# Kernel tuning notes

Measured on AMD Instinct MI355X. Metric: run time of the kernel, lower is better.

Reference implementation:

```python
import jax, jax.numpy as jnp
import numpy as np

TAU = 2.0       # spikingjelly LIFNode default tau
V_TH = 1.0      # default v_threshold
T_STEPS = 16
MAX_ACTION = 1.0
ALPHA = 4.0     # surrogate.Sigmoid default alpha

@jax.custom_vjp
def spike(x):
    # Heaviside(v - v_th) with sigmoid surrogate gradient
    return (x >= 0).astype(x.dtype)

def _spike_fwd(x):
    return spike(x), x

def _spike_bwd(x, g):
    s = jax.nn.sigmoid(ALPHA * x)
    return (g * ALPHA * s * (1.0 - s),)

spike.defvjp(_spike_fwd, _spike_bwd)

def setup_inputs() -> dict:
    key = jax.random.key(0)
    ks = jax.random.split(key, 7)
    B, S, H, A = 131072, 128, 256, 8
    def lin(k, out_d, in_d):
        return jax.random.normal(k, (out_d, in_d), jnp.float32) / np.sqrt(in_d)
    return {
        "state": jax.random.normal(ks[0], (B, S), jnp.float32),
        "W1": lin(ks[1], H, S),
        "b1": jax.random.normal(ks[2], (H,), jnp.float32) * 0.1,
        "W2": lin(ks[3], H, H),
        "b2": jax.random.normal(ks[4], (H,), jnp.float32) * 0.1,
        "W3": lin(ks[5], A, H),
        "b3": jax.random.normal(ks[6], (A,), jnp.float32) * 0.1,
    }

def reference(state, W1, b1, W2, b2, W3, b3):
    B = state.shape[0]
    H, A = W1.shape[0], W3.shape[0]
    # input current to layer 1 is identical every step -> hoist out of scan
    h1 = state @ W1.T + b1  # [B, 256]
    v0 = (jnp.zeros((B, H), state.dtype),
          jnp.zeros((B, H), state.dtype),
          jnp.zeros((B, A), state.dtype))

    def step(carry, _):
        v1, v2, v3 = carry
        # LIF 1: decay_input charge, hard reset to v_reset=0
        v1 = v1 + (h1 - v1) / TAU
        s1 = spike(v1 - V_TH)
        v1 = v1 * (1.0 - s1)
        # LIF 2
        h2 = s1 @ W2.T + b2
        v2 = v2 + (h2 - v2) / TAU
        s2 = spike(v2 - V_TH)
        v2 = v2 * (1.0 - s2)
        # NonSpiking LIF: charge only, no spike/reset
        h3 = s2 @ W3.T + b3
        v3 = v3 + (h3 - v3) / TAU
        return (v1, v2, v3), None

    (v1, v2, v3), _ = jax.lax.scan(step, v0, None, length=T_STEPS)
    return MAX_ACTION * jnp.tanh(v3)
```

## Files before the change

### kernel.cpp

```cpp
#include <hip/hip_runtime.h>
#include <hip/hip_bf16.h>
#include <math.h>

#define S_DIM 128
#define H_DIM 256
#define A_DIM 8
#define T_STEPS 16
#define BTW 16
#define EPS_BAND 2e-4f

typedef __attribute__((ext_vector_type(8))) short short8;
typedef __attribute__((ext_vector_type(4))) float f32x4;

__device__ inline unsigned short f32_to_bf16_rn(float f) {
    unsigned int u = __float_as_uint(f);
    return (unsigned short)((u + 0x7FFFu + ((u >> 16) & 1u)) >> 16);
}
__device__ inline float bf16_bits_to_f32(unsigned short b) {
    return __uint_as_float(((unsigned int)b) << 16);
}

__global__ __launch_bounds__(512, 2)
void snn_mfma(const float* __restrict__ state,
              const float* __restrict__ W1, const float* __restrict__ b1,
              const float* __restrict__ W2, const float* __restrict__ b2,
              const float* __restrict__ W3, const float* __restrict__ b3,
              float* __restrict__ out,
              unsigned int* __restrict__ gcount, unsigned int* __restrict__ glist,
              unsigned int listcap)
{
    __shared__ float lds_f[BTW * 260];
    __shared__ unsigned short s1t[BTW * 256];
    __shared__ float w3s[A_DIM * 260];
    __shared__ unsigned int flagw;

    const int tid = threadIdx.x;
    const int l   = tid & 63;
    const int w   = tid >> 6;
    const int cl  = l & 15;
    const int c8  = l >> 4;
    const long b0 = (long)blockIdx.x * BTW;

    if (tid == 0) flagw = 0;

    {
        const float4 v = reinterpret_cast<const float4*>(state + b0 * S_DIM)[tid];
        const int b = tid >> 5, k = (tid & 31) * 4;
        *reinterpret_cast<float4*>(&lds_f[b * S_DIM + k]) = v;
    }
    {
        const int a = tid >> 6, c = tid & 63;
        const float4 v = reinterpret_cast<const float4*>(W3)[tid];
        *reinterpret_cast<float4*>(&w3s[a * 260 + c * 4]) = v;
    }

    short8 bhi[2][8], bmid[2][8];
    #pragma unroll
    for (int nt = 0; nt < 2; ++nt) {
        const int n = w * 32 + nt * 16 + cl;
        #pragma unroll
        for (int ks = 0; ks < 8; ++ks) {
            const float* src = W2 + n * H_DIM + ks * 32 + c8 * 8;
            const float4 a0 = *reinterpret_cast<const float4*>(src);
            const float4 a1 = *reinterpret_cast<const float4*>(src + 4);
            const float wv[8] = {a0.x, a0.y, a0.z, a0.w, a1.x, a1.y, a1.z, a1.w};
            short8 hi8, mi8;
            #pragma unroll
            for (int e = 0; e < 8; ++e) {
                const unsigned short hb = f32_to_bf16_rn(wv[e]);
                const float rem = wv[e] - bf16_bits_to_f32(hb);
                hi8[e] = (short)hb;
                mi8[e] = (short)f32_to_bf16_rn(rem);
            }
            bhi[nt][ks] = hi8;
            bmid[nt][ks] = mi8;
        }
    }
    const float b2v0 = b2[w * 32 + cl];
    const float b2v1 = b2[w * 32 + 16 + cl];
    __syncthreads();

    const int n1 = tid & 255;
    const int bh = tid >> 8;
    unsigned int pat[4] = {0, 0, 0, 0};
    {
        double acc[8];
        #pragma unroll
        for (int i = 0; i < 8; ++i) acc[i] = 0.0;
        const float* w1p = W1 + n1 * S_DIM;
        for (int kq = 0; kq < 32; ++kq) {
            const float4 w4 = reinterpret_cast<const float4*>(w1p)[kq];
            const double wd0 = (double)w4.x, wd1 = (double)w4.y;
            const double wd2 = (double)w4.z, wd3 = (double)w4.w;
            #pragma unroll
            for (int b8 = 0; b8 < 8; ++b8) {
                const float4 s4 = *reinterpret_cast<const float4*>(
                    &lds_f[(bh * 8 + b8) * S_DIM + kq * 4]);
                double a = acc[b8];
                a = fma(wd0, (double)s4.x, a);
                a = fma(wd1, (double)s4.y, a);
                a = fma(wd2, (double)s4.z, a);
                a = fma(wd3, (double)s4.w, a);
                acc[b8] = a;
            }
        }
        const double b1d = (double)b1[n1];
        #pragma unroll
        for (int b8 = 0; b8 < 8; ++b8) {
            const double h1 = acc[b8] + b1d;
            double v = 0.0;
            unsigned int p = 0;
            for (int t = 0; t < T_STEPS; ++t) {
                v = v + (h1 - v) * 0.5;
                if (v >= 1.0) { p |= (1u << t); v = 0.0; }
            }
            pat[b8 >> 1] |= p << ((b8 & 1) * 16);
        }
    }

    f32x4 v2a = {0, 0, 0, 0}, v2b = {0, 0, 0, 0};
    f32x4 ua = {0, 0, 0, 0}, ub = {0, 0, 0, 0};
    unsigned int fl = 0;
    float ct = 0x1p-16f;

    #pragma unroll 1
    for (int t = 0; t < T_STEPS; ++t) {
        #pragma unroll
        for (int b8 = 0; b8 < 8; ++b8) {
            const int b = bh * 8 + b8;
            const unsigned int bit = (pat[b8 >> 1] >> ((b8 & 1) * 16 + t)) & 1u;
            s1t[b * 256 + (n1 ^ ((b & 7) << 3))] =
                bit ? (unsigned short)0x3F80 : (unsigned short)0;
        }
        __syncthreads();

        f32x4 acc0 = {0, 0, 0, 0}, acc1 = {0, 0, 0, 0};
        #pragma unroll
        for (int ks = 0; ks < 8; ++ks) {
            const int j0 = ks * 32 + c8 * 8;
            const short8 af = *reinterpret_cast<const short8*>(
                &s1t[cl * 256 + (j0 ^ ((cl & 7) << 3))]);
            acc0 = __builtin_amdgcn_mfma_f32_16x16x32_bf16(af, bhi[0][ks], acc0, 0, 0, 0);
            acc1 = __builtin_amdgcn_mfma_f32_16x16x32_bf16(af, bhi[1][ks], acc1, 0, 0, 0);
            acc0 = __builtin_amdgcn_mfma_f32_16x16x32_bf16(af, bmid[0][ks], acc0, 0, 0, 0);
            acc1 = __builtin_amdgcn_mfma_f32_16x16x32_bf16(af, bmid[1][ks], acc1, 0, 0, 0);
        }
        __syncthreads();

        #pragma unroll
        for (int r = 0; r < 4; ++r) {
            {
                const float h2 = acc0[r] + b2v0;
                float v = (v2a[r] + h2) * 0.5f;
                if (fabsf(v - 1.0f) < EPS_BAND) fl |= 1u << r;
                const bool sp = v >= 1.0f;
                v2a[r] = sp ? 0.0f : v;
                ua[r] += sp ? ct : 0.0f;
            }
            {
                const float h2 = acc1[r] + b2v1;
                float v = (v2b[r] + h2) * 0.5f;
                if (fabsf(v - 1.0f) < EPS_BAND) fl |= 1u << r;
                const bool sp = v >= 1.0f;
                v2b[r] = sp ? 0.0f : v;
                ub[r] += sp ? ct : 0.0f;
            }
        }
        ct *= 2.0f;
    }

    if (fl) atomicOr(&flagw, fl << (c8 * 4));

    #pragma unroll
    for (int r = 0; r < 4; ++r) {
        const int b = c8 * 4 + r;
        lds_f[b * 260 + w * 32 + cl]      = ua[r];
        lds_f[b * 260 + w * 32 + 16 + cl] = ub[r];
    }
    __syncthreads();

    if (tid < BTW * A_DIM) {
        const int b = tid >> 3, a = tid & 7;
        float s0 = 0, s1v = 0, s2v = 0, s3 = 0;
        #pragma unroll 8
        for (int kq = 0; kq < 64; ++kq) {
            const float4 uv = *reinterpret_cast<const float4*>(&lds_f[b * 260 + kq * 4]);
            const float4 wv = *reinterpret_cast<const float4*>(&w3s[a * 260 + kq * 4]);
            s0 = fmaf(uv.x, wv.x, s0);
            s1v = fmaf(uv.y, wv.y, s1v);
            s2v = fmaf(uv.z, wv.z, s2v);
            s3 = fmaf(uv.w, wv.w, s3);
        }
        const float v3 = (s0 + s1v) + (s2v + s3) + b3[a] * (1.0f - 0x1p-16f);
        out[(b0 + b) * A_DIM + a] = tanhf(v3);
    }

    if (tid < BTW) {
        if ((flagw >> tid) & 1u) {
            const unsigned int idx = atomicAdd(gcount, 1u);
            if (idx < listcap) glist[idx] = (unsigned int)(b0 + tid);
        }
    }
}

__global__ __launch_bounds__(512, 2)
void snn_fix(const float* __restrict__ state,
             const float* __restrict__ W1, const float* __restrict__ b1,
             const float* __restrict__ W2, const float* __restrict__ b2,
             const float* __restrict__ W3, const float* __restrict__ b3,
             float* __restrict__ out,
             const unsigned int* __restrict__ gcount,
             const unsigned int* __restrict__ glist,
             unsigned int listcap)
{
    __shared__ float  s1s[H_DIM];
    __shared__ double redh[H_DIM];
    __shared__ double uu[H_DIM];

    const int tid = threadIdx.x;
    const int n = tid & 255;
    const int kh = tid >> 8;
    unsigned int cnt = *gcount;
    if (cnt > listcap) cnt = listcap;
    if (cnt == 0) return;

    float4 w2f[32];
    #pragma unroll
    for (int q = 0; q < 32; ++q)
        w2f[q] = reinterpret_cast<const float4*>(W2 + n * H_DIM + kh * 128)[q];

    const double b1d = (double)b1[n];
    const double b2d = (double)b2[n];

    for (unsigned int i = blockIdx.x; i < cnt; i += gridDim.x) {
        const long be = (long)glist[i];

        double hp = 0.0;
        {
            const float* w1p = W1 + n * S_DIM + kh * 64;
            const float* stp = state + be * S_DIM + kh * 64;
            #pragma unroll
            for (int kq = 0; kq < 16; ++kq) {
                const float4 w4 = reinterpret_cast<const float4*>(w1p)[kq];
                const float4 s4 = reinterpret_cast<const float4*>(stp)[kq];
                hp = fma((double)w4.x, (double)s4.x, hp);
                hp = fma((double)w4.y, (double)s4.y, hp);
                hp = fma((double)w4.z, (double)s4.z, hp);
                hp = fma((double)w4.w, (double)s4.w, hp);
            }
        }
        if (kh) redh[n] = hp;
        __syncthreads();
        double h1 = 0.0, v1 = 0.0, v2 = 0.0, un = 0.0;
        if (!kh) h1 = hp + redh[n] + b1d;
        double ct = 0x1p-16;

        for (int t = 0; t < T_STEPS; ++t) {
            if (!kh) {
                v1 = v1 + (h1 - v1) * 0.5;
                const bool sp = (v1 >= 1.0);
                v1 = sp ? 0.0 : v1;
                s1s[n] = sp ? 1.0f : 0.0f;
            }
            __syncthreads();
            double h2p = 0.0;
            #pragma unroll
            for (int q = 0; q < 32; ++q) {
                const float4 w4 = w2f[q];
                const float4 s4 = *reinterpret_cast<const float4*>(&s1s[kh * 128 + q * 4]);
                h2p = fma((double)w4.x, (double)s4.x, h2p);
                h2p = fma((double)w4.y, (double)s4.y, h2p);
                h2p = fma((double)w4.z, (double)s4.z, h2p);
                h2p = fma((double)w4.w, (double)s4.w, h2p);
            }
            __syncthreads();
            if (kh) redh[n] = h2p;
            __syncthreads();
            if (!kh) {
                const double h2 = h2p + redh[n] + b2d;
                v2 = v2 + (h2 - v2) * 0.5;
                const bool sp = (v2 >= 1.0);
                v2 = sp ? 0.0 : v2;
                un += sp ? ct : 0.0;
            }
            ct *= 2.0;
        }
        if (!kh) uu[n] = un;
        __syncthreads();
        if (tid < A_DIM) {
            double d0 = 0, d1 = 0, d2 = 0, d3 = 0;
            const float* w3p = W3 + tid * H_DIM;
            for (int j = 0; j < H_DIM; j += 4) {
                d0 = fma((double)w3p[j],     uu[j],     d0);
                d1 = fma((double)w3p[j + 1], uu[j + 1], d1);
                d2 = fma((double)w3p[j + 2], uu[j + 2], d2);
                d3 = fma((double)w3p[j + 3], uu[j + 3], d3);
            }
            const double v3 = (d0 + d1) + (d2 + d3) + (double)b3[tid] * (1.0 - 0x1p-16);
            out[be * A_DIM + tid] = (float)tanh(v3);
        }
        __syncthreads();
    }
}

extern "C" void kernel_launch(void* const* d_in, const int* in_sizes, int n_in,
                              void* d_out, int out_size, void* d_ws, size_t ws_size,
                              hipStream_t stream)
{
    const float* state = (const float*)d_in[0];
    const float* W1    = (const float*)d_in[1];
    const float* b1    = (const float*)d_in[2];
    const float* W2    = (const float*)d_in[3];
    const float* b2    = (const float*)d_in[4];
    const float* W3    = (const float*)d_in[5];
    const float* b3    = (const float*)d_in[6];
    float* out = (float*)d_out;

    unsigned int* gcount = (unsigned int*)d_ws;
    unsigned int* glist  = (unsigned int*)d_ws + 4;
    const unsigned int listcap =
        (ws_size > 64) ? (unsigned int)((ws_size - 16) / 4) : 0;

    hipMemsetAsync(d_ws, 0, 16, stream);

    const int B = in_sizes[0] / S_DIM;

    snn_mfma<<<B / BTW, 512, 0, stream>>>(state, W1, b1, W2, b2, W3, b3,
                                          out, gcount, glist, listcap);
    snn_fix<<<2048, 512, 0, stream>>>(state, W1, b1, W2, b2, W3, b3,
                                      out, gcount, glist, listcap);
}
```

Baseline: 1.765 ms.

## Batch all timesteps into MFMA M-dimension, shrink batch tile to eight rows

Layer 1 spike patterns are stored in LDS, and the 16 timesteps become the M dimension of the layer-2 MFMA, two batch rows per pass. This replaces 16 per-timestep passes, each with two barriers, by 4 passes. The LIF-2 recurrence then runs serially per neuron after a transposed store through a skewed LDS buffer. The batch tile halves, which doubles the grid and adds LDS use, and W2 must still be split into bf16 hi/mid parts in every block.

```diff
diff --git a/kernel.cpp b/kernel.cpp
--- a/kernel.cpp
+++ b/kernel.cpp
@@ -6,10 +6,11 @@
 #define H_DIM 256
 #define A_DIM 8
 #define T_STEPS 16
-#define BTW 16
+#define BT 8
 #define EPS_BAND 2e-4f
 
 typedef __attribute__((ext_vector_type(8))) short short8;
+typedef __attribute__((ext_vector_type(8))) unsigned short ushort8;
 typedef __attribute__((ext_vector_type(4))) float f32x4;
 
 __device__ inline unsigned short f32_to_bf16_rn(float f) {
@@ -21,33 +22,31 @@
 }
 
 __global__ __launch_bounds__(512, 2)
-void snn_mfma(const float* __restrict__ state,
-              const float* __restrict__ W1, const float* __restrict__ b1,
-              const float* __restrict__ W2, const float* __restrict__ b2,
-              const float* __restrict__ W3, const float* __restrict__ b3,
-              float* __restrict__ out,
-              unsigned int* __restrict__ gcount, unsigned int* __restrict__ glist,
-              unsigned int listcap)
+void snn_tmfma(const float* __restrict__ state,
+               const float* __restrict__ W1, const float* __restrict__ b1,
+               const float* __restrict__ W2, const float* __restrict__ b2,
+               const float* __restrict__ W3, const float* __restrict__ b3,
+               float* __restrict__ out,
+               unsigned int* __restrict__ gcount, unsigned int* __restrict__ glist,
+               unsigned int listcap)
 {
-    __shared__ float lds_f[BTW * 260];
-    __shared__ unsigned short s1t[BTW * 256];
+    __shared__ float st_u[BT * 260];
+    __shared__ unsigned short pat[BT * 256];
+    __shared__ unsigned short atile[2][4096];
+    __shared__ float tbuf[8][2 * 512];
     __shared__ float w3s[A_DIM * 260];
     __shared__ unsigned int flagw;
 
     const int tid = threadIdx.x;
-    const int l   = tid & 63;
-    const int w   = tid >> 6;
-    const int cl  = l & 15;
-    const int c8  = l >> 4;
-    const long b0 = (long)blockIdx.x * BTW;
+    const int l = tid & 63, w = tid >> 6;
+    const int cl = l & 15, c8 = l >> 4;
+    const long b0 = (long)blockIdx.x * BT;
 
     if (tid == 0) flagw = 0;
 
-    {
-        const float4 v = reinterpret_cast<const float4*>(state + b0 * S_DIM)[tid];
-        const int b = tid >> 5, k = (tid & 31) * 4;
-        *reinterpret_cast<float4*>(&lds_f[b * S_DIM + k]) = v;
-    }
+    if (tid < 256)
+        reinterpret_cast<float4*>(st_u)[tid] =
+            reinterpret_cast<const float4*>(state + b0 * S_DIM)[tid];
     {
         const int a = tid >> 6, c = tid & 63;
         const float4 v = reinterpret_cast<const float4*>(W3)[tid];
@@ -76,115 +75,119 @@
             bmid[nt][ks] = mi8;
         }
     }
-    const float b2v0 = b2[w * 32 + cl];
-    const float b2v1 = b2[w * 32 + 16 + cl];
+    const float b2r = b2[w * 32 + (l & 31)];
     __syncthreads();
 
-    const int n1 = tid & 255;
-    const int bh = tid >> 8;
-    unsigned int pat[4] = {0, 0, 0, 0};
     {
-        double acc[8];
-        #pragma unroll
-        for (int i = 0; i < 8; ++i) acc[i] = 0.0;
+        const int n1 = tid & 255, bh = tid >> 8;
+        double acc[4] = {0.0, 0.0, 0.0, 0.0};
         const float* w1p = W1 + n1 * S_DIM;
+        #pragma unroll 4
         for (int kq = 0; kq < 32; ++kq) {
             const float4 w4 = reinterpret_cast<const float4*>(w1p)[kq];
             const double wd0 = (double)w4.x, wd1 = (double)w4.y;
             const double wd2 = (double)w4.z, wd3 = (double)w4.w;
             #pragma unroll
-            for (int b8 = 0; b8 < 8; ++b8) {
+            for (int b4 = 0; b4 < 4; ++b4) {
                 const float4 s4 = *reinterpret_cast<const float4*>(
-                    &lds_f[(bh * 8 + b8) * S_DIM + kq * 4]);
-                double a = acc[b8];
+                    &st_u[(bh * 4 + b4) * S_DIM + kq * 4]);
+                double a = acc[b4];
                 a = fma(wd0, (double)s4.x, a);
                 a = fma(wd1, (double)s4.y, a);
                 a = fma(wd2, (double)s4.z, a);
                 a = fma(wd3, (double)s4.w, a);
-                acc[b8] = a;
+                acc[b4] = a;
             }
         }
         const double b1d = (double)b1[n1];
         #pragma unroll
-        for (int b8 = 0; b8 < 8; ++b8) {
-            const double h1 = acc[b8] + b1d;
+        for (int b4 = 0; b4 < 4; ++b4) {
+            const double h1 = acc[b4] + b1d;
             double v = 0.0;
             unsigned int p = 0;
+            #pragma unroll
             for (int t = 0; t < T_STEPS; ++t) {
                 v = v + (h1 - v) * 0.5;
                 if (v >= 1.0) { p |= (1u << t); v = 0.0; }
             }
-            pat[b8 >> 1] |= p << ((b8 & 1) * 16);
-        }
-    }
-
-    f32x4 v2a = {0, 0, 0, 0}, v2b = {0, 0, 0, 0};
-    f32x4 ua = {0, 0, 0, 0}, ub = {0, 0, 0, 0};
-    unsigned int fl = 0;
-    float ct = 0x1p-16f;
+            pat[(bh * 4 + b4) * 256 + n1] = (unsigned short)p;
+        }
+    }
+    __syncthreads();
 
     #pragma unroll 1
-    for (int t = 0; t < T_STEPS; ++t) {
-        #pragma unroll
-        for (int b8 = 0; b8 < 8; ++b8) {
-            const int b = bh * 8 + b8;
-            const unsigned int bit = (pat[b8 >> 1] >> ((b8 & 1) * 16 + t)) & 1u;
-            s1t[b * 256 + (n1 ^ ((b & 7) << 3))] =
-                bit ? (unsigned short)0x3F80 : (unsigned short)0;
-        }
-        __syncthreads();
-
-        f32x4 acc0 = {0, 0, 0, 0}, acc1 = {0, 0, 0, 0};
+    for (int p2 = 0; p2 < 4; ++p2) {
+        {
+            const int t = l & 15, jq = l >> 4;
+            #pragma unroll
+            for (int bb = 0; bb < 2; ++bb) {
+                const int b = 2 * p2 + bb;
+                const ushort8 p8 = *reinterpret_cast<const ushort8*>(
+                    &pat[b * 256 + w * 32 + jq * 8]);
+                short8 af;
+                #pragma unroll
+                for (int e = 0; e < 8; ++e)
+                    af[e] = (short)((((unsigned int)p8[e] >> t) & 1u) ? 0x3F80 : 0);
+                *reinterpret_cast<short8*>(&atile[bb][(w * 64 + l) * 8]) = af;
+            }
+        }
+        __syncthreads();
+
+        f32x4 a00 = {0, 0, 0, 0}, a01 = {0, 0, 0, 0};
+        f32x4 a10 = {0, 0, 0, 0}, a11 = {0, 0, 0, 0};
         #pragma unroll
         for (int ks = 0; ks < 8; ++ks) {
-            const int j0 = ks * 32 + c8 * 8;
-            const short8 af = *reinterpret_cast<const short8*>(
-                &s1t[cl * 256 + (j0 ^ ((cl & 7) << 3))]);
-            acc0 = __builtin_amdgcn_mfma_f32_16x16x32_bf16(af, bhi[0][ks], acc0, 0, 0, 0);
-            acc1 = __builtin_amdgcn_mfma_f32_16x16x32_bf16(af, bhi[1][ks], acc1, 0, 0, 0);
-            acc0 = __builtin_amdgcn_mfma_f32_16x16x32_bf16(af, bmid[0][ks], acc0, 0, 0, 0);
-            acc1 = __builtin_amdgcn_mfma_f32_16x16x32_bf16(af, bmid[1][ks], acc1, 0, 0, 0);
-        }
-        __syncthreads();
-
-        #pragma unroll
-        for (int r = 0; r < 4; ++r) {
-            {
-                const float h2 = acc0[r] + b2v0;
-                float v = (v2a[r] + h2) * 0.5f;
-                if (fabsf(v - 1.0f) < EPS_BAND) fl |= 1u << r;
+            const short8 af0 = *reinterpret_cast<const short8*>(&atile[0][(ks * 64 + l) * 8]);
+            const short8 af1 = *reinterpret_cast<const short8*>(&atile[1][(ks * 64 + l) * 8]);
+            a00 = __builtin_amdgcn_mfma_f32_16x16x32_bf16(af0, bhi[0][ks], a00, 0, 0, 0);
+            a00 = __builtin_amdgcn_mfma_f32_16x16x32_bf16(af0, bmid[0][ks], a00, 0, 0, 0);
+            a01 = __builtin_amdgcn_mfma_f32_16x16x32_bf16(af0, bhi[1][ks], a01, 0, 0, 0);
+            a01 = __builtin_amdgcn_mfma_f32_16x16x32_bf16(af0, bmid[1][ks], a01, 0, 0, 0);
+            a10 = __builtin_amdgcn_mfma_f32_16x16x32_bf16(af1, bhi[0][ks], a10, 0, 0, 0);
+            a10 = __builtin_amdgcn_mfma_f32_16x16x32_bf16(af1, bmid[0][ks], a10, 0, 0, 0);
+            a11 = __builtin_amdgcn_mfma_f32_16x16x32_bf16(af1, bhi[1][ks], a11, 0, 0, 0);
+            a11 = __builtin_amdgcn_mfma_f32_16x16x32_bf16(af1, bmid[1][ks], a11, 0, 0, 0);
+        }
+
+        {
+            float* tb = tbuf[w];
+            #pragma unroll
+            for (int r = 0; r < 4; ++r) {
+                const int t = 4 * c8 + r;
+                tb[t * 32 + ((cl + 2 * t) & 31)]            = a00[r];
+                tb[t * 32 + ((16 + cl + 2 * t) & 31)]      = a01[r];
+                tb[512 + t * 32 + ((cl + 2 * t) & 31)]     = a10[r];
+                tb[512 + t * 32 + ((16 + cl + 2 * t) & 31)] = a11[r];
+            }
+        }
+        {
+            const int rm = l & 31, rbb = l >> 5;
+            const float* tb = tbuf[w] + rbb * 512;
+            float v2 = 0.0f, u = 0.0f, ct = 0x1p-16f;
+            unsigned int fl = 0;
+            #pragma unroll
+            for (int t = 0; t < T_STEPS; ++t) {
+                const float h2 = tb[t * 32 + ((rm + 2 * t) & 31)] + b2r;
+                const float v = (v2 + h2) * 0.5f;
+                if (fabsf(v - 1.0f) < EPS_BAND) fl = 1u;
                 const bool sp = v >= 1.0f;
-                v2a[r] = sp ? 0.0f : v;
-                ua[r] += sp ? ct : 0.0f;
-            }
-            {
-                const float h2 = acc1[r] + b2v1;
-                float v = (v2b[r] + h2) * 0.5f;
-                if (fabsf(v - 1.0f) < EPS_BAND) fl |= 1u << r;
-                const bool sp = v >= 1.0f;
-                v2b[r] = sp ? 0.0f : v;
-                ub[r] += sp ? ct : 0.0f;
-            }
-        }
-        ct *= 2.0f;
-    }
-
-    if (fl) atomicOr(&flagw, fl << (c8 * 4));
-
-    #pragma unroll
-    for (int r = 0; r < 4; ++r) {
-        const int b = c8 * 4 + r;
-        lds_f[b * 260 + w * 32 + cl]      = ua[r];
-        lds_f[b * 260 + w * 32 + 16 + cl] = ub[r];
-    }
-    __syncthreads();
-
-    if (tid < BTW * A_DIM) {
+                v2 = sp ? 0.0f : v;
+                u += sp ? ct : 0.0f;
+                ct *= 2.0f;
+            }
+            const int b = 2 * p2 + rbb;
+            st_u[b * 260 + w * 32 + rm] = u;
+            if (fl) atomicOr(&flagw, 1u << b);
+        }
+        __syncthreads();
+    }
+
+    if (tid < BT * A_DIM) {
         const int b = tid >> 3, a = tid & 7;
         float s0 = 0, s1v = 0, s2v = 0, s3 = 0;
         #pragma unroll 8
         for (int kq = 0; kq < 64; ++kq) {
-            const float4 uv = *reinterpret_cast<const float4*>(&lds_f[b * 260 + kq * 4]);
+            const float4 uv = *reinterpret_cast<const float4*>(&st_u[b * 260 + kq * 4]);
             const float4 wv = *reinterpret_cast<const float4*>(&w3s[a * 260 + kq * 4]);
             s0 = fmaf(uv.x, wv.x, s0);
             s1v = fmaf(uv.y, wv.y, s1v);
@@ -195,7 +198,7 @@
         out[(b0 + b) * A_DIM + a] = tanhf(v3);
     }
 
-    if (tid < BTW) {
+    if (tid < BT) {
         if ((flagw >> tid) & 1u) {
             const unsigned int idx = atomicAdd(gcount, 1u);
             if (idx < listcap) glist[idx] = (unsigned int)(b0 + tid);
@@ -325,7 +328,7 @@
 
     const int B = in_sizes[0] / S_DIM;
 
-    snn_mfma<<<B / BTW, 512, 0, stream>>>(state, W1, b1, W2, b2, W3, b3,
+    snn_tmfma<<<B / BT, 512, 0, stream>>>(state, W1, b1, W2, b2, W3, b3,
                                           out, gcount, glist, listcap);
     snn_fix<<<2048, 512, 0, stream>>>(state, W1, b1, W2, b2, W3, b3,
                                       out, gcount, glist, listcap);
```

After: 2.405 ms. 1.36x slower.
